# Kernel tuning notes

Hardware: AMD Instinct MI355X
Metric: run time of the kernel (lower is better)

## Reference

```python
import jax, jax.numpy as jnp
import numpy as np

B, N, D, H = 2, 1024, 768, 16
HD = D // H          # head_dim = 48
HID = 2 * D          # transition hidden = 1536
EPS = 1e-5


def _ln(x, w=None, b=None):
    m = x.mean(-1, keepdims=True)
    v = ((x - m) ** 2).mean(-1, keepdims=True)
    y = (x - m) * jax.lax.rsqrt(v + EPS)
    if w is not None:
        y = y * w
    if b is not None:
        y = y + b
    return y


def _adaln(a, s, snw, ssw, ssb, sbw):
    # a: LN without affine; s: LN with weight only; sigmoid-gated scale + bias
    an = _ln(a)
    sn = _ln(s, snw)
    return an * jax.nn.sigmoid(sn @ ssw + ssb) + sn @ sbw


def setup_inputs() -> dict:
    key = jax.random.key(0)
    ks = jax.random.split(key, 20)
    w = 0.02

    def nrm(k, shape, scale=1.0):
        return jax.random.normal(k, shape, jnp.float32) * scale

    return {
        "a": nrm(ks[0], (B, N, D)),
        "s": nrm(ks[1], (B, N, D)),
        "z": nrm(ks[2], (H, B, N, N), 0.1),  # pair bias, fed as attn mask
        "adaln1_snw": jnp.ones((D,), jnp.float32),
        "adaln1_ssw": nrm(ks[3], (D, D), w),
        "adaln1_ssb": jnp.zeros((D,), jnp.float32),
        "adaln1_sbw": nrm(ks[4], (D, D), w),
        "q_w": nrm(ks[5], (D, D), w),
        "q_b": jnp.zeros((D,), jnp.float32),
        "k_w": nrm(ks[6], (D, D), w),
        "v_w": nrm(ks[7], (D, D), w),
        "g_w": nrm(ks[8], (D, D), w),
        "o_w": nrm(ks[9], (D, D), w),
        "outproj_w": nrm(ks[10], (D, D), w),
        "outproj_b": jnp.zeros((D,), jnp.float32),
        "adaln2_snw": jnp.ones((D,), jnp.float32),
        "adaln2_ssw": nrm(ks[11], (D, D), w),
        "adaln2_ssb": jnp.zeros((D,), jnp.float32),
        "adaln2_sbw": nrm(ks[12], (D, D), w),
        "swish_w": nrm(ks[13], (D, 2 * HID), w),
        "a2b_w": nrm(ks[14], (D, HID), w),
        "b2a_w": nrm(ks[15], (HID, D), w),
        "op_w": nrm(ks[16], (D, D), w),
        "op_b": jnp.zeros((D,), jnp.float32),
    }


def reference(a, s, z,
              adaln1_snw, adaln1_ssw, adaln1_ssb, adaln1_sbw,
              q_w, q_b, k_w, v_w, g_w, o_w,
              outproj_w, outproj_b,
              adaln2_snw, adaln2_ssw, adaln2_ssb, adaln2_sbw,
              swish_w, a2b_w, b2a_w, op_w, op_b):
    # --- AdaLN then pair-bias attention ---
    b = _adaln(a, s, adaln1_snw, adaln1_ssw, adaln1_ssb, adaln1_sbw)

    q = (b @ q_w + q_b).reshape(B, N, H, HD)  # head split: outer H, inner HD
    k = (b @ k_w).reshape(B, N, H, HD)
    v = (b @ v_w).reshape(B, N, H, HD)

    scores = jnp.einsum('bqhd,bkhd->hbqk', q, k) * (HD ** -0.5) + z
    p = jax.nn.softmax(scores, axis=-1)
    o = jnp.einsum('hbqk,bkhd->bqhd', p, v).reshape(B, N, D)

    g = jax.nn.sigmoid(b @ g_w)
    x = (o * g) @ o_w

    # sigmoid-gated residual (AdaLN-zero-style output projection on s)
    a = a + jax.nn.sigmoid(s @ outproj_w + outproj_b) * x

    # --- ConditionedTransitionBlock ---
    a2 = _adaln(a, s, adaln2_snw, adaln2_ssw, adaln2_ssb, adaln2_sbw)
    sw = a2 @ swish_w                     # [B, N, 2*HID]
    u, gate = sw[..., :HID], sw[..., HID:]
    hidden = jax.nn.silu(gate) * u * (a2 @ a2b_w)
    t = jax.nn.sigmoid(s @ op_w + op_b) * (hidden @ b2a_w)

    return a + t
```

## Files before the change

kernel.cpp:

```cpp
#include <hip/hip_runtime.h>
#include <math.h>

constexpr int CB = 2, CN = 1024, CD = 768, CH = 16, CHD = 48, CHID = 1536;
constexpr int CT = CB * CN;
constexpr float CEPS = 1e-5f;

typedef __bf16 bf16_t;
typedef __bf16 bf16x8 __attribute__((ext_vector_type(8)));
typedef __bf16 bf16x4 __attribute__((ext_vector_type(4)));
typedef float  f32x4  __attribute__((ext_vector_type(4)));

__device__ __forceinline__ float sigf(float x) { return 1.f / (1.f + expf(-x)); }

__device__ __forceinline__ void gload16(const void* g, void* l) {
    __builtin_amdgcn_global_load_lds((const __attribute__((address_space(1))) void*)g,
                                     (__attribute__((address_space(3))) void*)l, 16, 0, 0);
}

__global__ __launch_bounds__(256) void ln_pre_k(
    const float* __restrict__ a, const float* __restrict__ s,
    const float* __restrict__ snw,
    float* __restrict__ an, bf16_t* __restrict__ snbf, bf16_t* __restrict__ sbf)
{
    __shared__ float r4[4][4];
    const int row = blockIdx.x;
    const int tid = threadIdx.x;
    const float* ar = a + (size_t)row * CD;
    const float* sr = s + (size_t)row * CD;

    float av[3], sv[3];
    float suma = 0.f, sqa = 0.f, sums = 0.f, sqs = 0.f;
#pragma unroll
    for (int j = 0; j < 3; ++j) {
        const int i = tid + j * 256;
        av[j] = ar[i]; sv[j] = sr[i];
        suma += av[j]; sqa += av[j] * av[j];
        sums += sv[j]; sqs += sv[j] * sv[j];
    }
#pragma unroll
    for (int o = 32; o > 0; o >>= 1) {
        suma += __shfl_down(suma, o, 64);
        sqa  += __shfl_down(sqa,  o, 64);
        sums += __shfl_down(sums, o, 64);
        sqs  += __shfl_down(sqs,  o, 64);
    }
    const int wv = tid >> 6;
    if ((tid & 63) == 0) { r4[0][wv] = suma; r4[1][wv] = sqa; r4[2][wv] = sums; r4[3][wv] = sqs; }
    __syncthreads();
    suma = r4[0][0] + r4[0][1] + r4[0][2] + r4[0][3];
    sqa  = r4[1][0] + r4[1][1] + r4[1][2] + r4[1][3];
    sums = r4[2][0] + r4[2][1] + r4[2][2] + r4[2][3];
    sqs  = r4[3][0] + r4[3][1] + r4[3][2] + r4[3][3];

    const float inv_d = 1.f / (float)CD;
    const float ma = suma * inv_d;
    const float ra = rsqrtf(sqa * inv_d - ma * ma + CEPS);
    const float ms = sums * inv_d;
    const float rs = rsqrtf(sqs * inv_d - ms * ms + CEPS);

#pragma unroll
    for (int j = 0; j < 3; ++j) {
        const int i = tid + j * 256;
        an[(size_t)row * CD + i]   = (av[j] - ma) * ra;
        snbf[(size_t)row * CD + i] = (bf16_t)((sv[j] - ms) * rs * snw[i]);
        if (sbf) sbf[(size_t)row * CD + i] = (bf16_t)sv[j];
    }
}

__global__ __launch_bounds__(256) void tcvt_k(
    const float* __restrict__ src, const int ld_src, const int col_ofs,
    bf16_t* __restrict__ dst, const int ld_dst, const int row_ofs)
{
    __shared__ float t[32][33];
    const int k0 = blockIdx.y * 32, n0 = blockIdx.x * 32;
    const int tx = threadIdx.x & 31, ty = threadIdx.x >> 5;
#pragma unroll
    for (int i = 0; i < 4; ++i)
        t[ty + 8 * i][tx] = src[(size_t)(k0 + ty + 8 * i) * ld_src + col_ofs + n0 + tx];
    __syncthreads();
#pragma unroll
    for (int i = 0; i < 4; ++i)
        dst[(size_t)(row_ofs + n0 + ty + 8 * i) * ld_dst + k0 + tx] = (bf16_t)t[tx][ty + 8 * i];
}

template<bool CBF16>
__global__ __launch_bounds__(256) void mgemm_k(
    const bf16_t* __restrict__ A, const int lda,
    const bf16_t* __restrict__ Bt, const int K,
    void* __restrict__ Cv, const int ldc)
{
    __shared__ __align__(16) bf16_t lA[2][128 * 32];
    __shared__ __align__(16) bf16_t lB[2][128 * 32];
    const int tid  = threadIdx.x;
    const int lane = tid & 63;
    const int m0 = blockIdx.y * 128;
    const int n0 = blockIdx.x * 128;
    const int wv = tid >> 6;
    const int wr = (wv >> 1) * 64;
    const int wc = (wv & 1) * 64;

    f32x4 acc[4][4] = {};

    const int r0 = tid >> 2,        kg0 = (tid & 3) * 8;
    const int r1 = (tid + 256) >> 2, kg1 = kg0;
    const int wbase = (tid & ~63) * 16;

#define STAGE(buf, kt)                                                                  \
    do {                                                                                \
        gload16(A  + (size_t)(m0 + r0) * lda + (kt) + kg0, (char*)lA[buf] + wbase);     \
        gload16(A  + (size_t)(m0 + r1) * lda + (kt) + kg1, (char*)lA[buf] + 4096 + wbase); \
        gload16(Bt + (size_t)(n0 + r0) * K   + (kt) + kg0, (char*)lB[buf] + wbase);     \
        gload16(Bt + (size_t)(n0 + r1) * K   + (kt) + kg1, (char*)lB[buf] + 4096 + wbase); \
    } while (0)

    const int nt = K >> 5;
    STAGE(0, 0);
    __syncthreads();

    const int afr = wr + (lane & 15);
    const int bfr_ = wc + (lane & 15);
    const int kof = (lane >> 4) * 8;

    for (int t = 0; t < nt; ++t) {
        const int buf = t & 1;
        if (t + 1 < nt) STAGE(buf ^ 1, (t + 1) << 5);
        bf16x8 af[4], bfv[4];
#pragma unroll
        for (int i = 0; i < 4; ++i) {
            af[i]  = *(const bf16x8*)&lA[buf][(afr + i * 16) * 32 + kof];
            bfv[i] = *(const bf16x8*)&lB[buf][(bfr_ + i * 16) * 32 + kof];
        }
#pragma unroll
        for (int mi = 0; mi < 4; ++mi)
#pragma unroll
            for (int ni = 0; ni < 4; ++ni)
                acc[mi][ni] = __builtin_amdgcn_mfma_f32_16x16x32_bf16(af[mi], bfv[ni], acc[mi][ni], 0, 0, 0);
        __syncthreads();
    }
#undef STAGE

    const int crow = m0 + wr + ((lane >> 4) << 2);
    const int ccol = n0 + wc + (lane & 15);
#pragma unroll
    for (int mi = 0; mi < 4; ++mi)
#pragma unroll
        for (int r = 0; r < 4; ++r) {
            const size_t ro = (size_t)(crow + mi * 16 + r) * ldc + ccol;
#pragma unroll
            for (int ni = 0; ni < 4; ++ni) {
                if (CBF16) ((bf16_t*)Cv)[ro + ni * 16] = (bf16_t)acc[mi][ni][r];
                else       ((float*)Cv)[ro + ni * 16]  = acc[mi][ni][r];
            }
        }
}

__global__ __launch_bounds__(256) void comb_adaln_k(
    const float* __restrict__ an, const bf16_t* __restrict__ ssb_mat,
    const float* __restrict__ bias, bf16_t* __restrict__ out)
{
    const int i4 = (blockIdx.x * 256 + threadIdx.x) * 4;
    const int row = i4 / CD, col = i4 - row * CD;
    const float4 anv = *(const float4*)&an[i4];
    const bf16x4 ssv = *(const bf16x4*)&ssb_mat[(size_t)row * 1536 + col];
    const bf16x4 sbv = *(const bf16x4*)&ssb_mat[(size_t)row * 1536 + 768 + col];
    const float4 bv  = *(const float4*)&bias[col];
    bf16x4 o;
    o[0] = (bf16_t)(anv.x * sigf((float)ssv[0] + bv.x) + (float)sbv[0]);
    o[1] = (bf16_t)(anv.y * sigf((float)ssv[1] + bv.y) + (float)sbv[1]);
    o[2] = (bf16_t)(anv.z * sigf((float)ssv[2] + bv.z) + (float)sbv[2]);
    o[3] = (bf16_t)(anv.w * sigf((float)ssv[3] + bv.w) + (float)sbv[3]);
    *(bf16x4*)&out[i4] = o;
}

__global__ __launch_bounds__(256) void gateadd_k(
    const float* __restrict__ base, const float* __restrict__ gates, const int g_ofs,
    const float* __restrict__ bias, const float* __restrict__ x, float* __restrict__ dst)
{
    const int i4 = (blockIdx.x * 256 + threadIdx.x) * 4;
    const int row = i4 / CD, col = i4 - row * CD;
    const float4 bv = *(const float4*)&base[i4];
    const float4 gv = *(const float4*)&gates[(size_t)row * 1536 + g_ofs + col];
    const float4 bi = *(const float4*)&bias[col];
    const float4 xv = *(const float4*)&x[i4];
    float4 o;
    o.x = bv.x + sigf(gv.x + bi.x) * xv.x;
    o.y = bv.y + sigf(gv.y + bi.y) * xv.y;
    o.z = bv.z + sigf(gv.z + bi.z) * xv.z;
    o.w = bv.w + sigf(gv.w + bi.w) * xv.w;
    *(float4*)&dst[i4] = o;
}

__global__ __launch_bounds__(256) void mlp_comb_k(
    const bf16_t* __restrict__ ugh, bf16_t* __restrict__ hidden)
{
    const int i4 = (blockIdx.x * 256 + threadIdx.x) * 4;
    const int row = i4 / CHID, col = i4 - row * CHID;
    const bf16x4 uv = *(const bf16x4*)&ugh[(size_t)row * 4608 + col];
    const bf16x4 gv = *(const bf16x4*)&ugh[(size_t)row * 4608 + 1536 + col];
    const bf16x4 hv = *(const bf16x4*)&ugh[(size_t)row * 4608 + 3072 + col];
    bf16x4 o;
#pragma unroll
    for (int j = 0; j < 4; ++j) {
        const float g = (float)gv[j];
        o[j] = (bf16_t)(g * sigf(g) * (float)uv[j] * (float)hv[j]);
    }
    *(bf16x4*)&hidden[i4] = o;
}

__global__ __launch_bounds__(256) void attn_k(
    const float* __restrict__ qkvg, const float* __restrict__ qb,
    const float* __restrict__ z, bf16_t* __restrict__ og)
{
    __shared__ float kls[64][52];
    __shared__ float vls[64][52];
    const int tid  = threadIdx.x;
    const int qb_i = blockIdx.x;
    const int h    = blockIdx.y;
    const int b    = blockIdx.z;
    const int r    = tid >> 2;
    const int quad = tid & 3;
    const int qrow = qb_i * 64 + r;
    const float scale = 0.14433756729740643f;

    float qreg[48];
    const float* qp = qkvg + (size_t)(b * CN + qrow) * 3072 + h * CHD;
#pragma unroll
    for (int j = 0; j < 12; ++j) {
        const float4 t4 = *(const float4*)(qp + j * 4);
        const float4 b4 = *(const float4*)(qb + h * CHD + j * 4);
        qreg[j * 4 + 0] = t4.x + b4.x; qreg[j * 4 + 1] = t4.y + b4.y;
        qreg[j * 4 + 2] = t4.z + b4.z; qreg[j * 4 + 3] = t4.w + b4.w;
    }
    float acc[48];
#pragma unroll
    for (int d = 0; d < 48; ++d) acc[d] = 0.f;
    float m = -1e30f, l = 0.f;

    const float* zbase = z + (((size_t)(h * CB + b)) * CN + qrow) * CN;
    const float* kbase = qkvg + 768  + h * CHD;
    const float* vbase = qkvg + 1536 + h * CHD;

    for (int kt = 0; kt < CN; kt += 64) {
        __syncthreads();
#pragma unroll
        for (int j = 0; j < 3; ++j) {
            const int idx = tid + j * 256;
            const int key = idx / 12;
            const int d4  = idx - key * 12;
            const size_t gofs = (size_t)(b * CN + kt + key) * 3072 + d4 * 4;
            *(float4*)&kls[key][d4 * 4] = *(const float4*)(kbase + gofs);
            *(float4*)&vls[key][d4 * 4] = *(const float4*)(vbase + gofs);
        }
        __syncthreads();

        float sc[16];
#pragma unroll
        for (int kk = 0; kk < 16; ++kk) {
            const int key = kk * 4 + quad;
            float dt = 0.f;
#pragma unroll
            for (int j = 0; j < 12; ++j) {
                const float4 k4 = *(const float4*)&kls[key][j * 4];
                dt = fmaf(qreg[j * 4 + 0], k4.x, dt);
                dt = fmaf(qreg[j * 4 + 1], k4.y, dt);
                dt = fmaf(qreg[j * 4 + 2], k4.z, dt);
                dt = fmaf(qreg[j * 4 + 3], k4.w, dt);
            }
            sc[kk] = dt * scale + zbase[kt + key];
        }
        float tmax = sc[0];
#pragma unroll
        for (int kk = 1; kk < 16; ++kk) tmax = fmaxf(tmax, sc[kk]);
        tmax = fmaxf(tmax, __shfl_xor(tmax, 1, 4));
        tmax = fmaxf(tmax, __shfl_xor(tmax, 2, 4));
        const float mnew = fmaxf(m, tmax);
        const float resc = expf(m - mnew);
        m = mnew;
        l *= resc;
#pragma unroll
        for (int d = 0; d < 48; ++d) acc[d] *= resc;

        float p[16]; float ps = 0.f;
#pragma unroll
        for (int kk = 0; kk < 16; ++kk) { p[kk] = expf(sc[kk] - mnew); ps += p[kk]; }
        l += ps;

#pragma unroll
        for (int kk = 0; kk < 16; ++kk) {
            const int key = kk * 4 + quad;
            const float pv = p[kk];
#pragma unroll
            for (int j = 0; j < 12; ++j) {
                const float4 v4 = *(const float4*)&vls[key][j * 4];
                acc[j * 4 + 0] = fmaf(pv, v4.x, acc[j * 4 + 0]);
                acc[j * 4 + 1] = fmaf(pv, v4.y, acc[j * 4 + 1]);
                acc[j * 4 + 2] = fmaf(pv, v4.z, acc[j * 4 + 2]);
                acc[j * 4 + 3] = fmaf(pv, v4.w, acc[j * 4 + 3]);
            }
        }
    }

    l += __shfl_xor(l, 1, 4);
    l += __shfl_xor(l, 2, 4);
    const float inv = 1.f / l;
#pragma unroll
    for (int d = 0; d < 48; ++d) {
        acc[d] += __shfl_xor(acc[d], 1, 4);
        acc[d] += __shfl_xor(acc[d], 2, 4);
    }
    if (quad == 0) {
        const float* gp = qkvg + (size_t)(b * CN + qrow) * 3072 + 2304 + h * CHD;
        bf16_t* op = og + (size_t)(b * CN + qrow) * CD + h * CHD;
#pragma unroll
        for (int j = 0; j < 12; ++j) {
            const float4 gv = *(const float4*)(gp + j * 4);
            bf16x4 o;
            o[0] = (bf16_t)(acc[j * 4 + 0] * inv * sigf(gv.x));
            o[1] = (bf16_t)(acc[j * 4 + 1] * inv * sigf(gv.y));
            o[2] = (bf16_t)(acc[j * 4 + 2] * inv * sigf(gv.z));
            o[3] = (bf16_t)(acc[j * 4 + 3] * inv * sigf(gv.w));
            *(bf16x4*)(op + j * 4) = o;
        }
    }
}

extern "C" void kernel_launch(void* const* d_in, const int* in_sizes, int n_in,
                              void* d_out, int out_size, void* d_ws, size_t ws_size,
                              hipStream_t stream)
{
    const float* a       = (const float*)d_in[0];
    const float* s       = (const float*)d_in[1];
    const float* z       = (const float*)d_in[2];
    const float* a1_snw  = (const float*)d_in[3];
    const float* a1_ssw  = (const float*)d_in[4];
    const float* a1_ssb  = (const float*)d_in[5];
    const float* a1_sbw  = (const float*)d_in[6];
    const float* q_w     = (const float*)d_in[7];
    const float* q_b     = (const float*)d_in[8];
    const float* k_w     = (const float*)d_in[9];
    const float* v_w     = (const float*)d_in[10];
    const float* g_w     = (const float*)d_in[11];
    const float* o_w     = (const float*)d_in[12];
    const float* outproj_w = (const float*)d_in[13];
    const float* outproj_b = (const float*)d_in[14];
    const float* a2_snw  = (const float*)d_in[15];
    const float* a2_ssw  = (const float*)d_in[16];
    const float* a2_ssb  = (const float*)d_in[17];
    const float* a2_sbw  = (const float*)d_in[18];
    const float* swish_w = (const float*)d_in[19];
    const float* a2b_w   = (const float*)d_in[20];
    const float* b2a_w   = (const float*)d_in[21];
    const float* op_w    = (const float*)d_in[22];
    const float* op_b    = (const float*)d_in[23];
    float* out = (float*)d_out;
    char*  wsb = (char*)d_ws;

    size_t off = 0;
    auto alloc = [&](size_t bytes) { char* p = wsb + off; off = (off + bytes + 255) & ~(size_t)255; return p; };
    float*  A_an    = (float*) alloc((size_t)CT * CD * 4);
    bf16_t* B_sn    = (bf16_t*)alloc((size_t)CT * CD * 2);
    bf16_t* C_sbf   = (bf16_t*)alloc((size_t)CT * CD * 2);
    bf16_t* D_ssb   = (bf16_t*)alloc((size_t)CT * 1536 * 2);
    bf16_t* E_act   = (bf16_t*)alloc((size_t)CT * CD * 2);
    char*   F_big   = (char*)  alloc((size_t)CT * 3072 * 4);
    float*  G_gates = (float*) alloc((size_t)CT * 1536 * 4);
    float*  H_anew  = (float*) alloc((size_t)CT * CD * 4);
    float*  J_x     = (float*) alloc((size_t)CT * CD * 4);
    bf16_t* W1t     = (bf16_t*)alloc((size_t)1536 * 768 * 2);
    bf16_t* W2t     = (bf16_t*)alloc((size_t)1536 * 768 * 2);
    bf16_t* Wqkvgt  = (bf16_t*)alloc((size_t)3072 * 768 * 2);
    bf16_t* Wgt     = (bf16_t*)alloc((size_t)1536 * 768 * 2);
    bf16_t* W3t     = (bf16_t*)alloc((size_t)4608 * 768 * 2);
    bf16_t* Wot     = (bf16_t*)alloc((size_t)768 * 768 * 2);
    bf16_t* Wb2at   = (bf16_t*)alloc((size_t)768 * 1536 * 2);
    float*  qkvg_f  = (float*)F_big;
    bf16_t* ugh_b   = (bf16_t*)F_big;
    bf16_t* hidden  = D_ssb;
    float*  y2      = A_an;

    const dim3 blk(256);
    const dim3 t88(24, 24);
    tcvt_k<<<t88, blk, 0, stream>>>(a1_ssw, 768, 0, W1t, 768, 0);
    tcvt_k<<<t88, blk, 0, stream>>>(a1_sbw, 768, 0, W1t, 768, 768);
    tcvt_k<<<t88, blk, 0, stream>>>(q_w, 768, 0, Wqkvgt, 768, 0);
    tcvt_k<<<t88, blk, 0, stream>>>(k_w, 768, 0, Wqkvgt, 768, 768);
    tcvt_k<<<t88, blk, 0, stream>>>(v_w, 768, 0, Wqkvgt, 768, 1536);
    tcvt_k<<<t88, blk, 0, stream>>>(g_w, 768, 0, Wqkvgt, 768, 2304);
    tcvt_k<<<t88, blk, 0, stream>>>(outproj_w, 768, 0, Wgt, 768, 0);
    tcvt_k<<<t88, blk, 0, stream>>>(op_w, 768, 0, Wgt, 768, 768);
    tcvt_k<<<t88, blk, 0, stream>>>(a2_ssw, 768, 0, W2t, 768, 0);
    tcvt_k<<<t88, blk, 0, stream>>>(a2_sbw, 768, 0, W2t, 768, 768);
    tcvt_k<<<dim3(48, 24), blk, 0, stream>>>(swish_w, 3072, 0,    W3t, 768, 0);
    tcvt_k<<<dim3(48, 24), blk, 0, stream>>>(swish_w, 3072, 1536, W3t, 768, 1536);
    tcvt_k<<<dim3(48, 24), blk, 0, stream>>>(a2b_w, 1536, 0,      W3t, 768, 3072);
    tcvt_k<<<t88, blk, 0, stream>>>(o_w, 768, 0, Wot, 768, 0);
    tcvt_k<<<dim3(24, 48), blk, 0, stream>>>(b2a_w, 768, 0, Wb2at, 1536, 0);

    const dim3 e768(CT * CD / 4 / 256);
    const dim3 e1536(CT * CHID / 4 / 256);
#define GRID(N) dim3((N) / 128, CT / 128)

    ln_pre_k<<<CT, blk, 0, stream>>>(a, s, a1_snw, A_an, B_sn, C_sbf);
    mgemm_k<true ><<<GRID(1536), blk, 0, stream>>>(B_sn, CD, W1t, 768, D_ssb, 1536);
    comb_adaln_k<<<e768, blk, 0, stream>>>(A_an, D_ssb, a1_ssb, E_act);
    mgemm_k<false><<<GRID(3072), blk, 0, stream>>>(E_act, CD, Wqkvgt, 768, qkvg_f, 3072);
    mgemm_k<false><<<GRID(1536), blk, 0, stream>>>(C_sbf, CD, Wgt, 768, G_gates, 1536);
    attn_k<<<dim3(CN / 64, CH, CB), blk, 0, stream>>>(qkvg_f, q_b, z, E_act);
    mgemm_k<false><<<GRID(768), blk, 0, stream>>>(E_act, CD, Wot, 768, J_x, 768);
    gateadd_k<<<e768, blk, 0, stream>>>(a, G_gates, 0, outproj_b, J_x, H_anew);
    ln_pre_k<<<CT, blk, 0, stream>>>(H_anew, s, a2_snw, A_an, B_sn, nullptr);
    mgemm_k<true ><<<GRID(1536), blk, 0, stream>>>(B_sn, CD, W2t, 768, D_ssb, 1536);
    comb_adaln_k<<<e768, blk, 0, stream>>>(A_an, D_ssb, a2_ssb, E_act);
    mgemm_k<true ><<<GRID(4608), blk, 0, stream>>>(E_act, CD, W3t, 768, ugh_b, 4608);
    mlp_comb_k<<<e1536, blk, 0, stream>>>(ugh_b, hidden);
    mgemm_k<false><<<GRID(768), blk, 0, stream>>>(hidden, CHID, Wb2at, 1536, y2, 768);
    gateadd_k<<<e768, blk, 0, stream>>>(H_anew, G_gates, 768, op_b, y2, out);
#undef GRID

    (void)in_sizes; (void)n_in; (void)out_size; (void)ws_size;
}
```

Before: 590.8 us.

## Batch weight transposes into one launch and give attention threads two query rows

The fifteen separate weight transpose/convert launches are merged into one kernel driven by a job table, so fourteen launch overheads go away. The attention kernel now has each group of 8 threads handle two query rows, and each thread covers 8 keys instead of 16. Each K/V value read from LDS is therefore reused for two rows, halving LDS traffic per FLOP. In exchange, register pressure roughly doubles for the q and accumulator arrays (launch bounds now ask for 2 blocks per unit), and there are more shuffle reductions.

```diff
diff --git a/kernel.cpp b/kernel.cpp
--- a/kernel.cpp
+++ b/kernel.cpp
@@ -67,12 +67,22 @@
     }
 }
 
-__global__ __launch_bounds__(256) void tcvt_k(
-    const float* __restrict__ src, const int ld_src, const int col_ofs,
-    bf16_t* __restrict__ dst, const int ld_dst, const int row_ofs)
+struct TJob { const float* src; bf16_t* dst; int ld_src, col_ofs, ld_dst, row_ofs, ntx, cnt; };
+struct TJobs { TJob j[15]; };
+
+__global__ __launch_bounds__(256) void tcvt_all_k(TJobs jobs)
 {
     __shared__ float t[32][33];
-    const int k0 = blockIdx.y * 32, n0 = blockIdx.x * 32;
+    int tb = blockIdx.x;
+    int ji = 0;
+    while (ji < 14 && tb >= jobs.j[ji].cnt) { tb -= jobs.j[ji].cnt; ++ji; }
+    const float* src = jobs.j[ji].src;
+    bf16_t* dst      = jobs.j[ji].dst;
+    const int ld_src = jobs.j[ji].ld_src, col_ofs = jobs.j[ji].col_ofs;
+    const int ld_dst = jobs.j[ji].ld_dst, row_ofs = jobs.j[ji].row_ofs;
+    const int ntx    = jobs.j[ji].ntx;
+    const int n0 = (tb % ntx) * 32;
+    const int k0 = (tb / ntx) * 32;
     const int tx = threadIdx.x & 31, ty = threadIdx.x >> 5;
 #pragma unroll
     for (int i = 0; i < 4; ++i)
@@ -207,7 +217,7 @@
     *(bf16x4*)&hidden[i4] = o;
 }
 
-__global__ __launch_bounds__(256) void attn_k(
+__global__ __launch_bounds__(256, 2) void attn_k(
     const float* __restrict__ qkvg, const float* __restrict__ qb,
     const float* __restrict__ z, bf16_t* __restrict__ og)
 {
@@ -217,26 +227,32 @@
     const int qb_i = blockIdx.x;
     const int h    = blockIdx.y;
     const int b    = blockIdx.z;
-    const int r    = tid >> 2;
-    const int quad = tid & 3;
-    const int qrow = qb_i * 64 + r;
+    const int p    = tid >> 3;
+    const int oct  = tid & 7;
+    const int r0   = qb_i * 64 + p * 2;
     const float scale = 0.14433756729740643f;
 
-    float qreg[48];
-    const float* qp = qkvg + (size_t)(b * CN + qrow) * 3072 + h * CHD;
-#pragma unroll
-    for (int j = 0; j < 12; ++j) {
-        const float4 t4 = *(const float4*)(qp + j * 4);
-        const float4 b4 = *(const float4*)(qb + h * CHD + j * 4);
-        qreg[j * 4 + 0] = t4.x + b4.x; qreg[j * 4 + 1] = t4.y + b4.y;
-        qreg[j * 4 + 2] = t4.z + b4.z; qreg[j * 4 + 3] = t4.w + b4.w;
-    }
-    float acc[48];
-#pragma unroll
-    for (int d = 0; d < 48; ++d) acc[d] = 0.f;
-    float m = -1e30f, l = 0.f;
-
-    const float* zbase = z + (((size_t)(h * CB + b)) * CN + qrow) * CN;
+    float qreg[2][48];
+#pragma unroll
+    for (int rr = 0; rr < 2; ++rr) {
+        const float* qp = qkvg + (size_t)(b * CN + r0 + rr) * 3072 + h * CHD;
+#pragma unroll
+        for (int j = 0; j < 12; ++j) {
+            const float4 t4 = *(const float4*)(qp + j * 4);
+            const float4 b4 = *(const float4*)(qb + h * CHD + j * 4);
+            qreg[rr][j * 4 + 0] = t4.x + b4.x; qreg[rr][j * 4 + 1] = t4.y + b4.y;
+            qreg[rr][j * 4 + 2] = t4.z + b4.z; qreg[rr][j * 4 + 3] = t4.w + b4.w;
+        }
+    }
+    float acc[2][48];
+#pragma unroll
+    for (int rr = 0; rr < 2; ++rr)
+#pragma unroll
+        for (int d = 0; d < 48; ++d) acc[rr][d] = 0.f;
+    float m[2] = {-1e30f, -1e30f}, l[2] = {0.f, 0.f};
+
+    const float* zb0 = z + (((size_t)(h * CB + b)) * CN + r0) * CN;
+    const float* zb1 = zb0 + CN;
     const float* kbase = qkvg + 768  + h * CHD;
     const float* vbase = qkvg + 1536 + h * CHD;
 
@@ -253,73 +269,96 @@
         }
         __syncthreads();
 
-        float sc[16];
-#pragma unroll
-        for (int kk = 0; kk < 16; ++kk) {
-            const int key = kk * 4 + quad;
-            float dt = 0.f;
+        float sc[2][8];
+#pragma unroll
+        for (int kk = 0; kk < 8; ++kk) {
+            const int key = kk * 8 + oct;
+            float d0 = 0.f, d1 = 0.f;
 #pragma unroll
             for (int j = 0; j < 12; ++j) {
                 const float4 k4 = *(const float4*)&kls[key][j * 4];
-                dt = fmaf(qreg[j * 4 + 0], k4.x, dt);
-                dt = fmaf(qreg[j * 4 + 1], k4.y, dt);
-                dt = fmaf(qreg[j * 4 + 2], k4.z, dt);
-                dt = fmaf(qreg[j * 4 + 3], k4.w, dt);
+                d0 = fmaf(qreg[0][j * 4 + 0], k4.x, d0);
+                d0 = fmaf(qreg[0][j * 4 + 1], k4.y, d0);
+                d0 = fmaf(qreg[0][j * 4 + 2], k4.z, d0);
+                d0 = fmaf(qreg[0][j * 4 + 3], k4.w, d0);
+                d1 = fmaf(qreg[1][j * 4 + 0], k4.x, d1);
+                d1 = fmaf(qreg[1][j * 4 + 1], k4.y, d1);
+                d1 = fmaf(qreg[1][j * 4 + 2], k4.z, d1);
+                d1 = fmaf(qreg[1][j * 4 + 3], k4.w, d1);
             }
-            sc[kk] = dt * scale + zbase[kt + key];
-        }
-        float tmax = sc[0];
-#pragma unroll
-        for (int kk = 1; kk < 16; ++kk) tmax = fmaxf(tmax, sc[kk]);
-        tmax = fmaxf(tmax, __shfl_xor(tmax, 1, 4));
-        tmax = fmaxf(tmax, __shfl_xor(tmax, 2, 4));
-        const float mnew = fmaxf(m, tmax);
-        const float resc = expf(m - mnew);
-        m = mnew;
-        l *= resc;
-#pragma unroll
-        for (int d = 0; d < 48; ++d) acc[d] *= resc;
-
-        float p[16]; float ps = 0.f;
-#pragma unroll
-        for (int kk = 0; kk < 16; ++kk) { p[kk] = expf(sc[kk] - mnew); ps += p[kk]; }
-        l += ps;
-
-#pragma unroll
-        for (int kk = 0; kk < 16; ++kk) {
-            const int key = kk * 4 + quad;
-            const float pv = p[kk];
+            sc[0][kk] = d0 * scale + zb0[kt + key];
+            sc[1][kk] = d1 * scale + zb1[kt + key];
+        }
+        float pr[2][8];
+#pragma unroll
+        for (int rr = 0; rr < 2; ++rr) {
+            float tmax = sc[rr][0];
+#pragma unroll
+            for (int kk = 1; kk < 8; ++kk) tmax = fmaxf(tmax, sc[rr][kk]);
+            tmax = fmaxf(tmax, __shfl_xor(tmax, 1, 8));
+            tmax = fmaxf(tmax, __shfl_xor(tmax, 2, 8));
+            tmax = fmaxf(tmax, __shfl_xor(tmax, 4, 8));
+            const float mnew = fmaxf(m[rr], tmax);
+            const float resc = expf(m[rr] - mnew);
+            m[rr] = mnew;
+            l[rr] *= resc;
+#pragma unroll
+            for (int d = 0; d < 48; ++d) acc[rr][d] *= resc;
+            float ps = 0.f;
+#pragma unroll
+            for (int kk = 0; kk < 8; ++kk) { pr[rr][kk] = expf(sc[rr][kk] - mnew); ps += pr[rr][kk]; }
+            l[rr] += ps;
+        }
+#pragma unroll
+        for (int kk = 0; kk < 8; ++kk) {
+            const int key = kk * 8 + oct;
+            const float p0 = pr[0][kk], p1 = pr[1][kk];
 #pragma unroll
             for (int j = 0; j < 12; ++j) {
                 const float4 v4 = *(const float4*)&vls[key][j * 4];
-                acc[j * 4 + 0] = fmaf(pv, v4.x, acc[j * 4 + 0]);
-                acc[j * 4 + 1] = fmaf(pv, v4.y, acc[j * 4 + 1]);
-                acc[j * 4 + 2] = fmaf(pv, v4.z, acc[j * 4 + 2]);
-                acc[j * 4 + 3] = fmaf(pv, v4.w, acc[j * 4 + 3]);
+                acc[0][j * 4 + 0] = fmaf(p0, v4.x, acc[0][j * 4 + 0]);
+                acc[0][j * 4 + 1] = fmaf(p0, v4.y, acc[0][j * 4 + 1]);
+                acc[0][j * 4 + 2] = fmaf(p0, v4.z, acc[0][j * 4 + 2]);
+                acc[0][j * 4 + 3] = fmaf(p0, v4.w, acc[0][j * 4 + 3]);
+                acc[1][j * 4 + 0] = fmaf(p1, v4.x, acc[1][j * 4 + 0]);
+                acc[1][j * 4 + 1] = fmaf(p1, v4.y, acc[1][j * 4 + 1]);
+                acc[1][j * 4 + 2] = fmaf(p1, v4.z, acc[1][j * 4 + 2]);
+                acc[1][j * 4 + 3] = fmaf(p1, v4.w, acc[1][j * 4 + 3]);
             }
         }
     }
 
-    l += __shfl_xor(l, 1, 4);
-    l += __shfl_xor(l, 2, 4);
-    const float inv = 1.f / l;
+#pragma unroll
+    for (int rr = 0; rr < 2; ++rr) {
+        l[rr] += __shfl_xor(l[rr], 1, 8);
+        l[rr] += __shfl_xor(l[rr], 2, 8);
+        l[rr] += __shfl_xor(l[rr], 4, 8);
+    }
 #pragma unroll
     for (int d = 0; d < 48; ++d) {
-        acc[d] += __shfl_xor(acc[d], 1, 4);
-        acc[d] += __shfl_xor(acc[d], 2, 4);
-    }
-    if (quad == 0) {
-        const float* gp = qkvg + (size_t)(b * CN + qrow) * 3072 + 2304 + h * CHD;
-        bf16_t* op = og + (size_t)(b * CN + qrow) * CD + h * CHD;
-#pragma unroll
-        for (int j = 0; j < 12; ++j) {
-            const float4 gv = *(const float4*)(gp + j * 4);
-            bf16x4 o;
-            o[0] = (bf16_t)(acc[j * 4 + 0] * inv * sigf(gv.x));
-            o[1] = (bf16_t)(acc[j * 4 + 1] * inv * sigf(gv.y));
-            o[2] = (bf16_t)(acc[j * 4 + 2] * inv * sigf(gv.z));
-            o[3] = (bf16_t)(acc[j * 4 + 3] * inv * sigf(gv.w));
-            *(bf16x4*)(op + j * 4) = o;
+#pragma unroll
+        for (int rr = 0; rr < 2; ++rr) {
+            acc[rr][d] += __shfl_xor(acc[rr][d], 1, 8);
+            acc[rr][d] += __shfl_xor(acc[rr][d], 2, 8);
+            acc[rr][d] += __shfl_xor(acc[rr][d], 4, 8);
+        }
+    }
+    if (oct == 0) {
+#pragma unroll
+        for (int rr = 0; rr < 2; ++rr) {
+            const float inv = 1.f / l[rr];
+            const float* gp = qkvg + (size_t)(b * CN + r0 + rr) * 3072 + 2304 + h * CHD;
+            bf16_t* op = og + (size_t)(b * CN + r0 + rr) * CD + h * CHD;
+#pragma unroll
+            for (int j = 0; j < 12; ++j) {
+                const float4 gv = *(const float4*)(gp + j * 4);
+                bf16x4 o;
+                o[0] = (bf16_t)(acc[rr][j * 4 + 0] * inv * sigf(gv.x));
+                o[1] = (bf16_t)(acc[rr][j * 4 + 1] * inv * sigf(gv.y));
+                o[2] = (bf16_t)(acc[rr][j * 4 + 2] * inv * sigf(gv.z));
+                o[3] = (bf16_t)(acc[rr][j * 4 + 3] * inv * sigf(gv.w));
+                *(bf16x4*)(op + j * 4) = o;
+            }
         }
     }
 }
@@ -379,22 +418,25 @@
     float*  y2      = A_an;
 
     const dim3 blk(256);
-    const dim3 t88(24, 24);
-    tcvt_k<<<t88, blk, 0, stream>>>(a1_ssw, 768, 0, W1t, 768, 0);
-    tcvt_k<<<t88, blk, 0, stream>>>(a1_sbw, 768, 0, W1t, 768, 768);
-    tcvt_k<<<t88, blk, 0, stream>>>(q_w, 768, 0, Wqkvgt, 768, 0);
-    tcvt_k<<<t88, blk, 0, stream>>>(k_w, 768, 0, Wqkvgt, 768, 768);
-    tcvt_k<<<t88, blk, 0, stream>>>(v_w, 768, 0, Wqkvgt, 768, 1536);
-    tcvt_k<<<t88, blk, 0, stream>>>(g_w, 768, 0, Wqkvgt, 768, 2304);
-    tcvt_k<<<t88, blk, 0, stream>>>(outproj_w, 768, 0, Wgt, 768, 0);
-    tcvt_k<<<t88, blk, 0, stream>>>(op_w, 768, 0, Wgt, 768, 768);
-    tcvt_k<<<t88, blk, 0, stream>>>(a2_ssw, 768, 0, W2t, 768, 0);
-    tcvt_k<<<t88, blk, 0, stream>>>(a2_sbw, 768, 0, W2t, 768, 768);
-    tcvt_k<<<dim3(48, 24), blk, 0, stream>>>(swish_w, 3072, 0,    W3t, 768, 0);
-    tcvt_k<<<dim3(48, 24), blk, 0, stream>>>(swish_w, 3072, 1536, W3t, 768, 1536);
-    tcvt_k<<<dim3(48, 24), blk, 0, stream>>>(a2b_w, 1536, 0,      W3t, 768, 3072);
-    tcvt_k<<<t88, blk, 0, stream>>>(o_w, 768, 0, Wot, 768, 0);
-    tcvt_k<<<dim3(24, 48), blk, 0, stream>>>(b2a_w, 768, 0, Wb2at, 1536, 0);
+
+    TJobs tj = {{
+        {a1_ssw,    W1t,    768,  0,    768,  0,    24, 576},
+        {a1_sbw,    W1t,    768,  0,    768,  768,  24, 576},
+        {q_w,       Wqkvgt, 768,  0,    768,  0,    24, 576},
+        {k_w,       Wqkvgt, 768,  0,    768,  768,  24, 576},
+        {v_w,       Wqkvgt, 768,  0,    768,  1536, 24, 576},
+        {g_w,       Wqkvgt, 768,  0,    768,  2304, 24, 576},
+        {outproj_w, Wgt,    768,  0,    768,  0,    24, 576},
+        {op_w,      Wgt,    768,  0,    768,  768,  24, 576},
+        {a2_ssw,    W2t,    768,  0,    768,  0,    24, 576},
+        {a2_sbw,    W2t,    768,  0,    768,  768,  24, 576},
+        {swish_w,   W3t,    3072, 0,    768,  0,    48, 1152},
+        {swish_w,   W3t,    3072, 1536, 768,  1536, 48, 1152},
+        {a2b_w,     W3t,    1536, 0,    768,  3072, 48, 1152},
+        {o_w,       Wot,    768,  0,    768,  0,    24, 576},
+        {b2a_w,     Wb2at,  768,  0,    1536, 0,    24, 1152},
+    }};
+    tcvt_all_k<<<dim3(10944), blk, 0, stream>>>(tj);
 
     const dim3 e768(CT * CD / 4 / 256);
     const dim3 e1536(CT * CHID / 4 / 256);
```

Result: slower. 657.3 us (+11.3%).
